# Kernel optimization log

Hardware: AMD Instinct MI355X
Metric: run time of the kernel (lower is better)

The kernel has to match this reference:

```python
import jax, jax.numpy as jnp
import numpy as np

D_K = 1  # global d_k from the source module


def setup_inputs() -> dict:
    key = jax.random.key(0)
    kq, kk, kv = jax.random.split(key, 3)
    B, H, S, Dv = 8, 8, 16384, 64
    Q = jax.random.normal(kq, (B, H, S, 1), dtype=jnp.float32)
    K = jax.random.normal(kk, (B, H, S, 1), dtype=jnp.float32)
    V = jax.random.normal(kv, (B, H, S, Dv), dtype=jnp.float32)
    return {"Q": Q, "K": K, "V": V}


def reference(Q, K, V):
    # Frobenius norm over the sequence axis (dim=2), unsqueezed at dim 3
    # K, Q: [B, H, S, 1] -> norm: [B, H, 1] -> [B, H, 1, 1]
    Kn = jnp.expand_dims(jnp.sqrt(jnp.sum(K * K, axis=2)), axis=3)
    Qn = jnp.expand_dims(jnp.sqrt(jnp.sum(Q * Q, axis=2)), axis=3)
    K = K / Kn
    Q = Q / Qn
    # Linear-attention reorder: (K^T V) first -> [B, H, 1, Dv]
    K_TV = jnp.einsum("bhsd,bhse->bhde", K, V) / np.float32(np.sqrt(D_K))
    # Q @ (K^T V) -> [B, H, S, Dv]
    context = jnp.einsum("bhsd,bhde->bhse", Q, K_TV)
    return context
```

## Files before the change

kernel.cpp:

```cpp
#include <hip/hip_runtime.h>
#include <math.h>

#define S_LEN 16384
#define DV    64
#define NBH   64
#define NBLK  16
#define CHUNK (S_LEN / NBLK)


__global__ __launch_bounds__(256) void stage1_partial_ktv(
    const float* __restrict__ K, const float* __restrict__ V,
    float* __restrict__ partial) {
    const int bh  = blockIdx.x >> 4;
    const int blk = blockIdx.x & 15;
    const int tid = threadIdx.x;
    const int e4  = tid & 15;
    const int sg  = tid >> 4;

    const float*  Kb = K + (size_t)bh * S_LEN;
    const float4* Vb = (const float4*)(V + (size_t)bh * S_LEN * DV);

    const int s0 = blk * CHUNK;
    float4 acc = make_float4(0.f, 0.f, 0.f, 0.f);
    #pragma unroll 4
    for (int i = 0; i < CHUNK / 16; ++i) {
        const int s = s0 + i * 16 + sg;
        const float  k = Kb[s];
        const float4 v = Vb[(size_t)s * 16 + e4];
        acc.x += k * v.x; acc.y += k * v.y;
        acc.z += k * v.z; acc.w += k * v.w;
    }

    __shared__ float4 red[16][16];
    red[sg][e4] = acc;
    __syncthreads();

    if (tid < DV) {
        const float* base = (const float*)red;
        float s = 0.f;
        #pragma unroll
        for (int p = 0; p < 16; ++p) s += base[p * DV + tid];
        partial[((size_t)bh * NBLK + blk) * DV + tid] = s;
    }
}

__global__ __launch_bounds__(256) void stage2_finalize(
    const float* __restrict__ Q, const float* __restrict__ K,
    const float* __restrict__ partial, float* __restrict__ fk) {
    const int bh  = blockIdx.x;
    const int tid = threadIdx.x;

    const float4* Q4 = (const float4*)(Q + (size_t)bh * S_LEN);
    const float4* K4 = (const float4*)(K + (size_t)bh * S_LEN);

    float qss = 0.f, kss = 0.f;
    for (int i = tid; i < S_LEN / 4; i += 256) {
        const float4 q = Q4[i];
        const float4 k = K4[i];
        qss += q.x * q.x + q.y * q.y + q.z * q.z + q.w * q.w;
        kss += k.x * k.x + k.y * k.y + k.z * k.z + k.w * k.w;
    }

    __shared__ float rq[256], rk[256];
    rq[tid] = qss; rk[tid] = kss;
    __syncthreads();
    #pragma unroll
    for (int off = 128; off > 0; off >>= 1) {
        if (tid < off) { rq[tid] += rq[tid + off]; rk[tid] += rk[tid + off]; }
        __syncthreads();
    }

    __shared__ float inv_norm;
    if (tid == 0) inv_norm = 1.0f / (sqrtf(rq[0]) * sqrtf(rk[0]));
    __syncthreads();

    if (tid < DV) {
        float s = 0.f;
        #pragma unroll
        for (int p = 0; p < NBLK; ++p)
            s += partial[((size_t)bh * NBLK + p) * DV + tid];
        fk[(size_t)bh * DV + tid] = s * inv_norm;
    }
}

__global__ __launch_bounds__(256) void stage3_outer(
    const float* __restrict__ Q, const float* __restrict__ fk,
    float4* __restrict__ out) {
    const size_t idx = (size_t)blockIdx.x * 256 + threadIdx.x;
    const int e4 = (int)(idx & 15);
    const int s  = (int)((idx >> 4) & (S_LEN - 1));
    const int bh = (int)(idx >> 18);

    const float  q = Q[(size_t)bh * S_LEN + s];
    const float4 f = ((const float4*)fk)[(size_t)bh * 16 + e4];
    out[idx] = make_float4(q * f.x, q * f.y, q * f.z, q * f.w);
}

extern "C" void kernel_launch(void* const* d_in, const int* in_sizes, int n_in,
                              void* d_out, int out_size, void* d_ws, size_t ws_size,
                              hipStream_t stream) {
    const float* Q = (const float*)d_in[0];
    const float* K = (const float*)d_in[1];
    const float* V = (const float*)d_in[2];
    float* out = (float*)d_out;

    float* partial = (float*)d_ws;
    float* fk      = partial + (size_t)NBH * NBLK * DV;

    stage1_partial_ktv<<<NBH * NBLK, 256, 0, stream>>>(K, V, partial);
    stage2_finalize<<<NBH, 256, 0, stream>>>(Q, K, partial, fk);

    const int n4 = NBH * S_LEN * (DV / 4);
    stage3_outer<<<n4 / 256, 256, 0, stream>>>(Q, fk, (float4*)out);
}
```

Before: 461.3 us.

## Fold Q/K norm reductions into stage1 and slim finalize; grid-stride stage3

Moves the Q and K sum-of-squares into the first kernel, which already streams K chunks. Each block now writes per-chunk partial norms, so the finalize kernel becomes a tiny 64-thread reduction over partials. That avoids the slow serial pass over Q and K with only 64 blocks. Stage3 now has each thread write four float4 outputs with a grid-sized stride, and the stage1 loop unroll goes from 4 to 8. The cost is extra shared-memory reduction steps and more barriers in stage1.

```diff
diff --git a/kernel.cpp b/kernel.cpp
--- a/kernel.cpp
+++ b/kernel.cpp
@@ -8,9 +8,10 @@
 #define CHUNK (S_LEN / NBLK)
 
 
-__global__ __launch_bounds__(256) void stage1_partial_ktv(
-    const float* __restrict__ K, const float* __restrict__ V,
-    float* __restrict__ partial) {
+__global__ __launch_bounds__(256) void stage1_partial(
+    const float* __restrict__ Q, const float* __restrict__ K,
+    const float* __restrict__ V,
+    float* __restrict__ pktv, float* __restrict__ pq, float* __restrict__ pk) {
     const int bh  = blockIdx.x >> 4;
     const int blk = blockIdx.x & 15;
     const int tid = threadIdx.x;
@@ -21,8 +22,16 @@
     const float4* Vb = (const float4*)(V + (size_t)bh * S_LEN * DV);
 
     const int s0 = blk * CHUNK;
+
+    const float4* Qc4 = (const float4*)(Q + (size_t)bh * S_LEN + s0);
+    const float4* Kc4 = (const float4*)(Kb + s0);
+    const float4 qv = Qc4[tid];
+    const float4 kv = Kc4[tid];
+    float q2 = qv.x * qv.x + qv.y * qv.y + qv.z * qv.z + qv.w * qv.w;
+    float k2 = kv.x * kv.x + kv.y * kv.y + kv.z * kv.z + kv.w * kv.w;
+
     float4 acc = make_float4(0.f, 0.f, 0.f, 0.f);
-    #pragma unroll 4
+    #pragma unroll 8
     for (int i = 0; i < CHUNK / 16; ++i) {
         const int s = s0 + i * 16 + sg;
         const float  k = Kb[s];
@@ -32,7 +41,9 @@
     }
 
     __shared__ float4 red[16][16];
+    __shared__ float rq[256], rk[256];
     red[sg][e4] = acc;
+    rq[tid] = q2; rk[tid] = k2;
     __syncthreads();
 
     if (tid < DV) {
@@ -40,60 +51,59 @@
         float s = 0.f;
         #pragma unroll
         for (int p = 0; p < 16; ++p) s += base[p * DV + tid];
-        partial[((size_t)bh * NBLK + blk) * DV + tid] = s;
+        pktv[((size_t)bh * NBLK + blk) * DV + tid] = s;
     }
-}
-
-__global__ __launch_bounds__(256) void stage2_finalize(
-    const float* __restrict__ Q, const float* __restrict__ K,
-    const float* __restrict__ partial, float* __restrict__ fk) {
-    const int bh  = blockIdx.x;
-    const int tid = threadIdx.x;
-
-    const float4* Q4 = (const float4*)(Q + (size_t)bh * S_LEN);
-    const float4* K4 = (const float4*)(K + (size_t)bh * S_LEN);
-
-    float qss = 0.f, kss = 0.f;
-    for (int i = tid; i < S_LEN / 4; i += 256) {
-        const float4 q = Q4[i];
-        const float4 k = K4[i];
-        qss += q.x * q.x + q.y * q.y + q.z * q.z + q.w * q.w;
-        kss += k.x * k.x + k.y * k.y + k.z * k.z + k.w * k.w;
-    }
-
-    __shared__ float rq[256], rk[256];
-    rq[tid] = qss; rk[tid] = kss;
-    __syncthreads();
     #pragma unroll
     for (int off = 128; off > 0; off >>= 1) {
         if (tid < off) { rq[tid] += rq[tid + off]; rk[tid] += rk[tid + off]; }
         __syncthreads();
     }
-
-    __shared__ float inv_norm;
-    if (tid == 0) inv_norm = 1.0f / (sqrtf(rq[0]) * sqrtf(rk[0]));
-    __syncthreads();
-
-    if (tid < DV) {
-        float s = 0.f;
-        #pragma unroll
-        for (int p = 0; p < NBLK; ++p)
-            s += partial[((size_t)bh * NBLK + p) * DV + tid];
-        fk[(size_t)bh * DV + tid] = s * inv_norm;
+    if (tid == 0) {
+        pq[bh * NBLK + blk] = rq[0];
+        pk[bh * NBLK + blk] = rk[0];
     }
 }
 
+__global__ __launch_bounds__(64) void stage2_finalize(
+    const float* __restrict__ pktv, const float* __restrict__ pq,
+    const float* __restrict__ pk, float* __restrict__ fk) {
+    const int bh  = blockIdx.x;
+    const int tid = threadIdx.x;
+
+    float s = 0.f;
+    #pragma unroll
+    for (int p = 0; p < NBLK; ++p)
+        s += pktv[((size_t)bh * NBLK + p) * DV + tid];
+
+    __shared__ float inv_norm;
+    if (tid == 0) {
+        float qss = 0.f, kss = 0.f;
+        #pragma unroll
+        for (int p = 0; p < NBLK; ++p) { qss += pq[bh * NBLK + p]; kss += pk[bh * NBLK + p]; }
+        inv_norm = 1.0f / (sqrtf(qss) * sqrtf(kss));
+    }
+    __syncthreads();
+
+    fk[(size_t)bh * DV + tid] = s * inv_norm;
+}
+
+#define S3_BLOCKS 16384
 __global__ __launch_bounds__(256) void stage3_outer(
     const float* __restrict__ Q, const float* __restrict__ fk,
     float4* __restrict__ out) {
-    const size_t idx = (size_t)blockIdx.x * 256 + threadIdx.x;
-    const int e4 = (int)(idx & 15);
-    const int s  = (int)((idx >> 4) & (S_LEN - 1));
-    const int bh = (int)(idx >> 18);
-
-    const float  q = Q[(size_t)bh * S_LEN + s];
-    const float4 f = ((const float4*)fk)[(size_t)bh * 16 + e4];
-    out[idx] = make_float4(q * f.x, q * f.y, q * f.z, q * f.w);
+    const size_t stride = (size_t)S3_BLOCKS * 256;
+    size_t idx = (size_t)blockIdx.x * 256 + threadIdx.x;
+    const size_t n4 = (size_t)NBH * S_LEN * (DV / 4);
+    #pragma unroll
+    for (int it = 0; it < 4; ++it, idx += stride) {
+        const int e4 = (int)(idx & 15);
+        const int s  = (int)((idx >> 4) & (S_LEN - 1));
+        const int bh = (int)(idx >> 18);
+        const float  q = Q[(size_t)bh * S_LEN + s];
+        const float4 f = ((const float4*)fk)[(size_t)bh * 16 + e4];
+        out[idx] = make_float4(q * f.x, q * f.y, q * f.z, q * f.w);
+    }
+    (void)n4;
 }
 
 extern "C" void kernel_launch(void* const* d_in, const int* in_sizes, int n_in,
@@ -104,12 +114,12 @@
     const float* V = (const float*)d_in[2];
     float* out = (float*)d_out;
 
-    float* partial = (float*)d_ws;
-    float* fk      = partial + (size_t)NBH * NBLK * DV;
+    float* pktv = (float*)d_ws;
+    float* pq   = pktv + (size_t)NBH * NBLK * DV;
+    float* pk   = pq + NBH * NBLK;
+    float* fk   = pk + NBH * NBLK;
 
-    stage1_partial_ktv<<<NBH * NBLK, 256, 0, stream>>>(K, V, partial);
-    stage2_finalize<<<NBH, 256, 0, stream>>>(Q, K, partial, fk);
-
-    const int n4 = NBH * S_LEN * (DV / 4);
-    stage3_outer<<<n4 / 256, 256, 0, stream>>>(Q, fk, (float4*)out);
+    stage1_partial<<<NBH * NBLK, 256, 0, stream>>>(Q, K, V, pktv, pq, pk);
+    stage2_finalize<<<NBH, 64, 0, stream>>>(pktv, pq, pk, fk);
+    stage3_outer<<<S3_BLOCKS, 256, 0, stream>>>(Q, fk, (float4*)out);
 }
```

Result: no change. 469.5 us (+1.8%).
